# Optimization experiments

Hardware: AMD Instinct MI355X
Metric: run time of the kernel (lower is better)

The kernel has to match this reference:

```python
import jax, jax.numpy as jnp
import numpy as np

H = 128   # hidden_size
E = 300   # embedding_dim
VOC = 32000
B, TP, TC = 8, 160, 160
D2 = 2 * H  # bidirectional feature dim


def gru_dir(x, Wih, Whh, bih, bhh, reverse):
    # x: [B,T,I] -> hidden states [B,T,Hs]; torch GRU gate order (r,z,n)
    Hs = Whh.shape[1]
    xg = jnp.einsum('bti,gi->btg', x, Wih) + bih  # [B,T,3Hs]
    if reverse:
        xg = xg[:, ::-1]
    def step(h, xt):
        gh = h @ Whh.T + bhh
        xr, xz, xn = jnp.split(xt, 3, axis=-1)
        hr, hz, hn = jnp.split(gh, 3, axis=-1)
        r = jax.nn.sigmoid(xr + hr)
        z = jax.nn.sigmoid(xz + hz)
        n = jnp.tanh(xn + r * hn)
        h = (1.0 - z) * n + z * h
        return h, h
    h0 = jnp.zeros((x.shape[0], Hs), x.dtype)
    _, hs = jax.lax.scan(step, h0, jnp.swapaxes(xg, 0, 1))
    hs = jnp.swapaxes(hs, 0, 1)
    if reverse:
        hs = hs[:, ::-1]
    return hs


def bigru(x, Wf, Uf, bif, bhf, Wb, Ub, bib, bhb):
    return jnp.concatenate([
        gru_dir(x, Wf, Uf, bif, bhf, False),
        gru_dir(x, Wb, Ub, bib, bhb, True)], axis=-1)


def setup_inputs() -> dict:
    key = jax.random.key(0)
    ks = iter(jax.random.split(key, 64))
    def rn(shape, s=0.05):
        return jax.random.normal(next(ks), shape, jnp.float32) * s
    inp = {}
    inp['text_a'] = jax.random.randint(next(ks), (B, TP), 0, VOC)
    inp['text_b'] = jax.random.randint(next(ks), (B, TC), 0, VOC)
    inp['emb'] = rn((VOC, E), 0.1)
    for pfx, ins in [('p', E), ('c', E), ('a', 6 * D2)]:
        for d in ('f', 'b'):
            inp[pfx + '_Wih_' + d] = rn((3 * H, ins))
            inp[pfx + '_Whh_' + d] = rn((3 * H, H))
            inp[pfx + '_bih_' + d] = jnp.zeros((3 * H,), jnp.float32)
            inp[pfx + '_bhh_' + d] = jnp.zeros((3 * H,), jnp.float32)
    inp['Wc1'] = rn((H, D2)); inp['Wc2'] = rn((H, D2)); inp['Vc'] = rn((H,))
    inp['Wb'] = rn((D2, D2))
    inp['Wd'] = rn((H, D2)); inp['Vd'] = rn((H,))
    inp['Wm'] = rn((H, D2)); inp['Vm'] = rn((H,))
    inp['Ws'] = rn((H, D2)); inp['Vs'] = rn((H,))
    inp['Wp'] = rn((H, D2)); inp['Vp'] = rn((H,))
    inp['W1'] = rn((H, D2)); inp['W2'] = rn((H, D2)); inp['Vv'] = rn((H,))
    inp['Wout'] = rn((2, D2)); inp['bout'] = jnp.zeros((2,), jnp.float32)
    return inp


def _forward(text_a, text_b, emb,
             p_Wih_f, p_Whh_f, p_bih_f, p_bhh_f, p_Wih_b, p_Whh_b, p_bih_b, p_bhh_b,
             c_Wih_f, c_Whh_f, c_bih_f, c_bhh_f, c_Wih_b, c_Whh_b, c_bih_b, c_bhh_b,
             a_Wih_f, a_Whh_f, a_bih_f, a_bhh_f, a_Wih_b, a_Whh_b, a_bih_b, a_bhh_b,
             Wc1, Wc2, Vc, Wb, Wd, Vd, Wm, Vm, Ws, Vs, Wp, Vp, W1, W2, Vv, Wout, bout):
    hp = bigru(emb[text_a], p_Wih_f, p_Whh_f, p_bih_f, p_bhh_f,
               p_Wih_b, p_Whh_b, p_bih_b, p_bhh_b)          # [B,Tp,2H]
    hc = bigru(emb[text_b], c_Wih_f, c_Whh_f, c_bih_f, c_bhh_f,
               c_Wih_b, c_Whh_b, c_bih_b, c_bhh_b)          # [B,Tc,2H]
    # concat (additive) attention: [B,Tc,Tp,H]
    s = jnp.tanh((hp @ Wc1.T)[:, None] + (hc @ Wc2.T)[:, :, None])
    a_cat = jax.nn.softmax(s @ Vc, axis=2)                   # [B,Tc,Tp]
    concat_rep = jnp.einsum('bct,btd->bcd', a_cat, hp)
    # bilinear attention
    a_bil = jax.nn.softmax(jnp.einsum('bcd,btd->bct', hc, hp @ Wb.T), axis=2)
    bil_rep = jnp.einsum('bct,btd->bcd', a_bil, hp)
    # dot / minus attention on [B,Tc,Tp,2H] broadcasts
    hp4 = hp[:, None]; hc4 = hc[:, :, None]
    a_dot = jax.nn.softmax(jnp.tanh((hp4 * hc4) @ Wd.T) @ Vd, axis=2)
    dot_rep = jnp.einsum('bct,btd->bcd', a_dot, hp)
    a_min = jax.nn.softmax(jnp.tanh((hp4 - hc4) @ Wm.T) @ Vm, axis=2)
    minus_rep = jnp.einsum('bct,btd->bcd', a_min, hp)
    # self attention on hc: [B,Tc,Tc,2H]
    a_self = jax.nn.softmax(jnp.tanh((hc[:, None] * hc[:, :, None]) @ Ws.T) @ Vs, axis=2)
    self_rep = jnp.einsum('bct,btd->bcd', a_self, hc)
    agg_in = jnp.concatenate([hc, self_rep, concat_rep, dot_rep, bil_rep, minus_rep], axis=-1)
    agg = bigru(agg_in, a_Wih_f, a_Whh_f, a_bih_f, a_bhh_f,
                a_Wih_b, a_Whh_b, a_bih_b, a_bhh_b)          # [B,Tc,2H]
    # pooled passage rep
    ap = jax.nn.softmax(jnp.tanh(hp @ Wp.T) @ Vp, axis=-1)   # [B,Tp]
    rp = jnp.einsum('bt,btd->bd', ap, hp)                    # [B,2H]
    # final attention over aggregation (note: no tanh, faithful to source)
    sc = (agg @ W1.T + (rp @ W2.T)[:, None]) @ Vv            # [B,Tc]
    ac = jax.nn.softmax(sc, axis=-1)
    rc = jnp.einsum('bc,bcd->bd', ac, agg)                   # [B,2H]
    return rc @ Wout.T + bout                                # [B,2] logits


def reference(text_a, text_b, emb,
              p_Wih_f, p_Whh_f, p_bih_f, p_bhh_f, p_Wih_b, p_Whh_b, p_bih_b, p_bhh_b,
              c_Wih_f, c_Whh_f, c_bih_f, c_bhh_f, c_Wih_b, c_Whh_b, c_bih_b, c_bhh_b,
              a_Wih_f, a_Whh_f, a_bih_f, a_bhh_f, a_Wih_b, a_Whh_b, a_bih_b, a_bhh_b,
              Wc1, Wc2, Vc, Wb, Wd, Vd, Wm, Vm, Ws, Vs, Wp, Vp, W1, W2, Vv, Wout, bout):
    return _forward(text_a, text_b, emb,
                    p_Wih_f, p_Whh_f, p_bih_f, p_bhh_f, p_Wih_b, p_Whh_b, p_bih_b, p_bhh_b,
                    c_Wih_f, c_Whh_f, c_bih_f, c_bhh_f, c_Wih_b, c_Whh_b, c_bih_b, c_bhh_b,
                    a_Wih_f, a_Whh_f, a_bih_f, a_bhh_f, a_Wih_b, a_Whh_b, a_bih_b, a_bhh_b,
                    Wc1, Wc2, Vc, Wb, Wd, Vd, Wm, Vm, Ws, Vs, Wp, Vp, W1, W2, Vv, Wout, bout)
```

## Files before the change

kernel.cpp:

```cpp
#include <hip/hip_runtime.h>

#define BB 8
#define TT 160
#define EE 300
#define HH 128
#define D2 256
#define G3 384
#define PSTR 40

typedef __attribute__((ext_vector_type(8))) short bf16x8;
typedef __attribute__((ext_vector_type(4))) float floatx4;

__device__ inline float fsigmoid(float x){ return 1.f/(1.f+__expf(-x)); }
__device__ inline float ftanh(float x){ return 2.f*fsigmoid(2.f*x) - 1.f; }

__device__ inline void split2(float x, unsigned short& hi, unsigned short& lo){
  unsigned ux = __float_as_uint(x);
  hi = (unsigned short)(ux>>16);
  float r = x - __uint_as_float(ux & 0xFFFF0000u);
  lo = (unsigned short)(__float_as_uint(r)>>16);
}

__global__ __launch_bounds__(256) void k_embed(const int* ta, const int* tb,
    const float* emb, float* ep, float* ec){
  const int idx = blockIdx.x*256 + threadIdx.x;
  const int per = BB*TT*EE;
  if (idx < per){
    const int e = idx % EE, bt = idx / EE;
    ep[idx] = emb[(long)ta[bt]*EE + e];
  } else {
    const int j = idx - per;
    const int e = j % EE, bt = j / EE;
    ec[j] = emb[(long)tb[bt]*EE + e];
  }
}

__global__ __launch_bounds__(256) void k_splitarr(const float* a, const float* b, int n,
    unsigned short* ahi, unsigned short* alo, unsigned short* bhi, unsigned short* blo){
  const int idx = blockIdx.x*256 + threadIdx.x;
  if (idx < n){
    split2(a[idx], ahi[idx], alo[idx]);
    split2(b[idx], bhi[idx], blo[idx]);
  }
}

struct SplitJob { const float* W; unsigned short* hi; unsigned short* lo; int n; int K; int Kp; };
struct SplitJobs { SplitJob j[12]; };

__global__ __launch_bounds__(256) void k_splitw(SplitJobs jobs){
  const SplitJob J = jobs.j[blockIdx.z];
  const int idx = blockIdx.x*256 + threadIdx.x;
  if (idx >= J.n) return;
  const int row = idx / J.Kp, k = idx - row*J.Kp;
  const float v = (k < J.K) ? J.W[(long)row*J.K + k] : 0.f;
  split2(v, J.hi[idx], J.lo[idx]);
}

struct GemmSJob {
  const float* A; const unsigned short* Whi; const unsigned short* Wlo; const float* bias;
  float* C; int N; int K; int Kp;
};
struct GemmSJobs { GemmSJob j[6]; };

__global__ __launch_bounds__(256) void k_gemmS(GemmSJobs jobs){
  const GemmSJob J = jobs.j[blockIdx.z];
  const int tid = threadIdx.x;
  const int lane = tid & 63, w = tid >> 6;
  const int l15 = lane & 15, q = lane >> 4;
  const int n0 = blockIdx.x * 64;
  if (n0 >= J.N) return;
  const int K = J.K, Kp = J.Kp;
  const long mrow = blockIdx.y*64 + w*16 + l15;
  const float* Arow = J.A + mrow*K;
  floatx4 acc[4];
  #pragma unroll
  for (int t=0;t<4;t++) acc[t] = (floatx4)0.f;
  const int nch = (K+31)>>5;
  for (int kc=0; kc<nch; kc++){
    const int k0 = kc<<5;
    const int kb = k0 + q*8;
    float av[8];
    if (k0+32 <= K){
      const floatx4 a0 = *(const floatx4*)(Arow+kb);
      const floatx4 a1 = *(const floatx4*)(Arow+kb+4);
      av[0]=a0[0];av[1]=a0[1];av[2]=a0[2];av[3]=a0[3];
      av[4]=a1[0];av[5]=a1[1];av[6]=a1[2];av[7]=a1[3];
    } else {
      #pragma unroll
      for (int j=0;j<8;j++){ const int k=kb+j; av[j] = (k<K)? Arow[k] : 0.f; }
    }
    union { bf16x8 v; unsigned short u[8]; } ahi, alo;
    #pragma unroll
    for (int j=0;j<8;j++) split2(av[j], ahi.u[j], alo.u[j]);
    #pragma unroll
    for (int t=0;t<4;t++){
      const int n = n0 + t*16 + l15;
      const long wo = (long)n*Kp + kb;
      union { bf16x8 v; uint4 d; } whi, wlo;
      whi.d = *(const uint4*)(J.Whi + wo);
      wlo.d = *(const uint4*)(J.Wlo + wo);
      acc[t] = __builtin_amdgcn_mfma_f32_16x16x32_bf16(ahi.v, whi.v, acc[t], 0,0,0);
      acc[t] = __builtin_amdgcn_mfma_f32_16x16x32_bf16(ahi.v, wlo.v, acc[t], 0,0,0);
      acc[t] = __builtin_amdgcn_mfma_f32_16x16x32_bf16(alo.v, whi.v, acc[t], 0,0,0);
    }
  }
  const long rbase = blockIdx.y*64 + w*16 + q*4;
  #pragma unroll
  for (int t=0;t<4;t++){
    const int n = n0 + t*16 + l15;
    const float bv = J.bias ? J.bias[n] : 0.f;
    #pragma unroll
    for (int r=0;r<4;r++)
      J.C[(rbase+r)*(long)J.N + n] = acc[t][r] + bv;
  }
}

struct GruJob { const float* xg; const float* Whh; const float* bhh; float* out; int ocol; int rev; };
struct GruJobs { GruJob j[4]; };

__global__ __launch_bounds__(256,1) void k_gru(GruJobs jobs){
  const GruJob J = jobs.j[blockIdx.y];
  const int bi = blockIdx.x;
  const int tid = threadIdx.x;
  const int j = tid >> 1, p = tid & 1;
  __shared__ float h_sh[2][HH];
  float wr[64], wz[64], wn[64];
  {
    const float* r0 = J.Whh + (long)j*HH + p*64;
    const float* z0 = J.Whh + (long)(HH+j)*HH + p*64;
    const float* n0 = J.Whh + (long)(2*HH+j)*HH + p*64;
    #pragma unroll
    for (int k=0;k<64;k+=4){
      *(floatx4*)&wr[k] = *(const floatx4*)(r0+k);
      *(floatx4*)&wz[k] = *(const floatx4*)(z0+k);
      *(floatx4*)&wn[k] = *(const floatx4*)(n0+k);
    }
  }
  float bhr=0.f,bhz=0.f,bhn=0.f, xr=0.f,xz=0.f,xn=0.f;
  if (p==0){
    bhr = J.bhh[j]; bhz = J.bhh[HH+j]; bhn = J.bhh[2*HH+j];
    const int t0 = J.rev ? (TT-1) : 0;
    const float* xgp = J.xg + ((long)bi*TT + t0)*G3;
    xr = xgp[j]; xz = xgp[HH+j]; xn = xgp[2*HH+j];
  }
  ((float*)h_sh)[tid] = 0.f;
  float hreg = 0.f;
  __syncthreads();
  for (int t=0;t<TT;t++){
    const int tt = J.rev ? (TT-1-t) : t;
    const int buf = t & 1;
    const float cxr=xr, cxz=xz, cxn=xn;
    if (p==0 && t+1 < TT){
      const int tn = J.rev ? (TT-2-t) : (t+1);
      const float* xgp = J.xg + ((long)bi*TT + tn)*G3;
      xr = xgp[j]; xz = xgp[HH+j]; xn = xgp[2*HH+j];
    }
    float ar0=0.f,ar1=0.f, az0=0.f,az1=0.f, an0=0.f,an1=0.f;
    #pragma unroll
    for (int k=0;k<64;k+=8){
      const floatx4 h0 = *(const floatx4*)&h_sh[buf][p*64+k];
      const floatx4 h1 = *(const floatx4*)&h_sh[buf][p*64+k+4];
      ar0 += wr[k]*h0[0] + wr[k+1]*h0[1] + wr[k+2]*h0[2] + wr[k+3]*h0[3];
      az0 += wz[k]*h0[0] + wz[k+1]*h0[1] + wz[k+2]*h0[2] + wz[k+3]*h0[3];
      an0 += wn[k]*h0[0] + wn[k+1]*h0[1] + wn[k+2]*h0[2] + wn[k+3]*h0[3];
      ar1 += wr[k+4]*h1[0] + wr[k+5]*h1[1] + wr[k+6]*h1[2] + wr[k+7]*h1[3];
      az1 += wz[k+4]*h1[0] + wz[k+5]*h1[1] + wz[k+6]*h1[2] + wz[k+7]*h1[3];
      an1 += wn[k+4]*h1[0] + wn[k+5]*h1[1] + wn[k+6]*h1[2] + wn[k+7]*h1[3];
    }
    float ar = ar0+ar1, az = az0+az1, an = an0+an1;
    ar += __shfl_xor(ar,1);
    az += __shfl_xor(az,1);
    an += __shfl_xor(an,1);
    if (p==0){
      const float gr = fsigmoid(cxr + ar + bhr);
      const float gz = fsigmoid(cxz + az + bhz);
      const float gn = ftanh  (cxn + gr*(an + bhn));
      const float h = (1.f-gz)*gn + gz*hreg;
      hreg = h;
      h_sh[1-buf][j] = h;
      J.out[((long)bi*TT + tt)*D2 + J.ocol + j] = h;
    }
    __syncthreads();
  }
}

__device__ inline float block_softmax160(float s, int tid, float* red){
  float m = s;
  #pragma unroll
  for (int o=32;o>0;o>>=1) m = fmaxf(m, __shfl_xor(m,o));
  if ((tid&63)==0) red[tid>>6] = m;
  __syncthreads();
  m = fmaxf(fmaxf(red[0],red[1]), fmaxf(red[2],red[3]));
  const float p = (tid<TT) ? __expf(s-m) : 0.f;
  float t = p;
  #pragma unroll
  for (int o=32;o>0;o>>=1) t += __shfl_xor(t,o);
  if ((tid&63)==0) red[4+(tid>>6)] = t;
  __syncthreads();
  const float sum = red[4]+red[5]+red[6]+red[7];
  return p / sum;
}

__device__ inline float block_softmax160_512(float s, int tid, float* red){
  float m = s;
  #pragma unroll
  for (int o=32;o>0;o>>=1) m = fmaxf(m, __shfl_xor(m,o));
  if ((tid&63)==0) red[tid>>6] = m;
  __syncthreads();
  m = red[0];
  #pragma unroll
  for (int i=1;i<8;i++) m = fmaxf(m, red[i]);
  const float p = (tid<TT) ? __expf(s-m) : 0.f;
  float t = p;
  #pragma unroll
  for (int o=32;o>0;o>>=1) t += __shfl_xor(t,o);
  if ((tid&63)==0) red[8+(tid>>6)] = t;
  __syncthreads();
  float sum = red[8];
  #pragma unroll
  for (int i=1;i<8;i++) sum += red[8+i];
  return p / sum;
}

struct PairJob { const unsigned short* Phi; const unsigned short* Plo;
                 const float* Q; const float* W; const float* V; float* a_out; };

__global__ __launch_bounds__(512) void k_pairattn(PairJob j0, PairJob j1){
  const PairJob J = blockIdx.z ? j1 : j0;
  const int b = blockIdx.y, c = blockIdx.x;
  const int tid = threadIdx.x;
  const int lane = tid & 63, w = tid >> 6;
  const int l15 = lane & 15, q = lane >> 4;
  __shared__ unsigned short Pb[2*2*160*PSTR];
  __shared__ float Qs[D2];
  __shared__ float sc_sh[TT];
  __shared__ float red[16];
  if (tid < D2) Qs[tid] = J.Q[((long)b*TT + c)*D2 + tid];
  if (tid < TT) sc_sh[tid] = 0.f;
  const long pbase = (long)b*TT*D2;

  int s_hl[5], s_t[5], s_d4[5];
  #pragma unroll
  for (int r=0;r<5;r++){
    const int idx = tid + r*512;
    const int hl = (idx >= 1280) ? 1 : 0;
    const int e4 = idx - hl*1280;
    s_hl[r] = hl; s_t[r] = e4 >> 3; s_d4[r] = e4 & 7;
  }
  uint2 stg[5];
  #pragma unroll
  for (int r=0;r<5;r++){
    const unsigned short* src = (s_hl[r] ? J.Plo : J.Phi) + pbase + (long)s_t[r]*D2 + s_d4[r]*4;
    stg[r] = *(const uint2*)src;
  }
  const float* Wbase = J.W + (long)(w*16 + l15)*D2;
  floatx4 wv0 = *(const floatx4*)(Wbase + q*8);
  floatx4 wv1 = *(const floatx4*)(Wbase + q*8 + 4);
  #pragma unroll
  for (int r=0;r<5;r++)
    *(uint2*)&Pb[((0*2 + s_hl[r])*160 + s_t[r])*PSTR + s_d4[r]*4] = stg[r];
  __syncthreads();

  floatx4 acc[10];
  #pragma unroll
  for (int nt=0;nt<10;nt++) acc[nt] = (floatx4)0.f;

  for (int kc=0; kc<8; kc++){
    const floatx4 wc0 = wv0, wc1 = wv1;
    if (kc < 7){
      wv0 = *(const floatx4*)(Wbase + (kc+1)*32 + q*8);
      wv1 = *(const floatx4*)(Wbase + (kc+1)*32 + q*8 + 4);
      #pragma unroll
      for (int r=0;r<5;r++){
        const unsigned short* src = (s_hl[r] ? J.Plo : J.Phi) + pbase + (long)s_t[r]*D2 + (kc+1)*32 + s_d4[r]*4;
        stg[r] = *(const uint2*)src;
      }
    }
    const int d0 = kc*32 + q*8;
    const floatx4 q0 = *(const floatx4*)&Qs[d0];
    const floatx4 q1 = *(const floatx4*)&Qs[d0+4];
    union { bf16x8 v; unsigned short u[8]; } ah, al;
    #pragma unroll
    for (int j=0;j<4;j++){
      split2(wc0[j]*q0[j], ah.u[j],   al.u[j]);
      split2(wc1[j]*q1[j], ah.u[4+j], al.u[4+j]);
    }
    const int buf = kc & 1;
    #pragma unroll
    for (int nt=0;nt<10;nt++){
      const int t = nt*16 + l15;
      union { bf16x8 v; } bh, bl;
      bh.v = *(const bf16x8*)&Pb[((buf*2+0)*160 + t)*PSTR + q*8];
      bl.v = *(const bf16x8*)&Pb[((buf*2+1)*160 + t)*PSTR + q*8];
      acc[nt] = __builtin_amdgcn_mfma_f32_16x16x32_bf16(ah.v, bh.v, acc[nt], 0,0,0);
      acc[nt] = __builtin_amdgcn_mfma_f32_16x16x32_bf16(ah.v, bl.v, acc[nt], 0,0,0);
      acc[nt] = __builtin_amdgcn_mfma_f32_16x16x32_bf16(al.v, bh.v, acc[nt], 0,0,0);
    }
    if (kc < 7){
      const int nbuf = 1 - buf;
      #pragma unroll
      for (int r=0;r<5;r++)
        *(uint2*)&Pb[((nbuf*2 + s_hl[r])*160 + s_t[r])*PSTR + s_d4[r]*4] = stg[r];
      __syncthreads();
    }
  }

  float vreg[4];
  #pragma unroll
  for (int r=0;r<4;r++) vreg[r] = J.V[w*16 + q*4 + r];
  #pragma unroll
  for (int nt=0;nt<10;nt++){
    float pp = 0.f;
    #pragma unroll
    for (int r=0;r<4;r++) pp += vreg[r]*ftanh(acc[nt][r]);
    pp += __shfl_xor(pp,16);
    pp += __shfl_xor(pp,32);
    if (q==0) atomicAdd(&sc_sh[nt*16 + l15], pp);
  }
  __syncthreads();
  const float s = (tid<TT)? sc_sh[tid] : -INFINITY;
  const float a = block_softmax160_512(s, tid, red);
  if (tid < TT) J.a_out[((long)b*TT + c)*TT + tid] = a;
}

struct AddJob { const float* up; const float* uc; const float* V; float sgn; float* a_out; };

__global__ __launch_bounds__(256) void k_addattn(AddJob j0, AddJob j1){
  const AddJob J = blockIdx.z ? j1 : j0;
  const int b = blockIdx.y, c = blockIdx.x, tid = threadIdx.x;
  __shared__ float ucc[HH];
  __shared__ float vv[HH];
  __shared__ float red[8];
  if (tid < HH){
    ucc[tid] = J.sgn * J.uc[((long)b*TT + c)*HH + tid];
    vv[tid] = J.V[tid];
  }
  __syncthreads();
  float s = -INFINITY;
  if (tid < TT){
    const float* ur = J.up + ((long)b*TT + tid)*HH;
    float a0 = 0.f;
    #pragma unroll 4
    for (int k=0;k<HH;k++) a0 += vv[k]*ftanh(ur[k]+ucc[k]);
    s = a0;
  }
  const float a = block_softmax160(s, tid, red);
  if (tid < TT) J.a_out[((long)b*TT + c)*TT + tid] = a;
}

__global__ __launch_bounds__(256) void k_bilattn(const float* hc, const float* hpWb, float* a_out){
  const int b = blockIdx.y, c = blockIdx.x, tid = threadIdx.x;
  __shared__ float hcc[D2];
  __shared__ float red[8];
  if (tid < D2) hcc[tid] = hc[((long)b*TT + c)*D2 + tid];
  __syncthreads();
  float s = -INFINITY;
  if (tid < TT){
    const float* pr = hpWb + ((long)b*TT + tid)*D2;
    float a0 = 0.f;
    #pragma unroll 4
    for (int k=0;k<D2;k++) a0 += hcc[k]*pr[k];
    s = a0;
  }
  const float a = block_softmax160(s, tid, red);
  if (tid < TT) a_out[((long)b*TT + c)*TT + tid] = a;
}

__global__ __launch_bounds__(256) void k_rep(const float* hp, const float* hc,
    const float* acat, const float* abil, const float* adot, const float* amin, const float* aself,
    float* aggin){
  const int b = blockIdx.y, c = blockIdx.x, tid = threadIdx.x;
  __shared__ float a5[5][TT];
  {
    const long base = ((long)b*TT + c)*TT;
    for (int i=tid;i<5*TT;i+=256){
      const int which = i/TT, t = i - which*TT;
      const float* p = which==0? acat : which==1? abil : which==2? adot : which==3? amin : aself;
      a5[which][t] = p[base + t];
    }
  }
  __syncthreads();
  const float* hpb = hp + (long)b*TT*D2 + tid;
  const float* hcb = hc + (long)b*TT*D2 + tid;
  float r0=0.f,r1=0.f,r2=0.f,r3=0.f,r4=0.f;
  for (int t=0;t<TT;t++){
    const float vp = hpb[(long)t*D2];
    const float vc = hcb[(long)t*D2];
    r0 += a5[0][t]*vp;
    r1 += a5[1][t]*vp;
    r2 += a5[2][t]*vp;
    r3 += a5[3][t]*vp;
    r4 += a5[4][t]*vc;
  }
  float* o = aggin + ((long)b*TT + c)*(6*D2);
  o[tid]        = hc[((long)b*TT + c)*D2 + tid];
  o[D2 + tid]   = r4;
  o[2*D2 + tid] = r0;
  o[3*D2 + tid] = r2;
  o[4*D2 + tid] = r1;
  o[5*D2 + tid] = r3;
}

__global__ __launch_bounds__(256) void k_tail1(const float* upP, const float* Vp,
    const float* hp, float* rp){
  const int b = blockIdx.x, tid = threadIdx.x;
  __shared__ float vv[HH];
  __shared__ float ap_sh[TT];
  __shared__ float red[8];
  if (tid<HH) vv[tid] = Vp[tid];
  __syncthreads();
  float s = -INFINITY;
  if (tid<TT){
    const float* ur = upP + ((long)b*TT + tid)*HH;
    float a0=0.f;
    #pragma unroll 4
    for (int k=0;k<HH;k++) a0 += vv[k]*ftanh(ur[k]);
    s = a0;
  }
  const float a = block_softmax160(s, tid, red);
  if (tid<TT) ap_sh[tid] = a;
  __syncthreads();
  float acc = 0.f;
  const float* hpb = hp + (long)b*TT*D2 + tid;
  for (int t=0;t<TT;t++) acc += ap_sh[t]*hpb[(long)t*D2];
  rp[b*D2 + tid] = acc;
}

__global__ __launch_bounds__(256) void k_tail2(const float* aggW1, const float* agg, const float* rp,
    const float* W2, const float* Vv, const float* Wout, const float* bout,
    float* out){
  const int b = blockIdx.x, tid = threadIdx.x;
  __shared__ float rpw[HH];
  __shared__ float ac_sh[TT];
  __shared__ float rc_sh[D2];
  __shared__ float red[8];
  if (tid < HH){
    float a0=0.f;
    const float* wr2 = W2 + (long)tid*D2;
    const float* rr = rp + b*D2;
    for (int d=0; d<D2; d++) a0 += wr2[d]*rr[d];
    rpw[tid] = a0;
  }
  __syncthreads();
  float s = -INFINITY;
  if (tid < TT){
    const float* ar = aggW1 + ((long)b*TT + tid)*HH;
    float a0=0.f;
    for (int k=0;k<HH;k++) a0 += Vv[k]*(ar[k] + rpw[k]);
    s = a0;
  }
  const float a = block_softmax160(s, tid, red);
  if (tid < TT) ac_sh[tid] = a;
  __syncthreads();
  float rc=0.f;
  const float* ab = agg + (long)b*TT*D2 + tid;
  for (int t=0;t<TT;t++) rc += ac_sh[t]*ab[(long)t*D2];
  rc_sh[tid] = rc;
  __syncthreads();
  if (tid < 2){
    float o = bout[tid];
    const float* wr = Wout + (long)tid*D2;
    for (int d=0; d<D2; d++) o += wr[d]*rc_sh[d];
    out[b*2 + tid] = o;
  }
}

extern "C" void kernel_launch(void* const* d_in, const int* in_sizes, int n_in,
                              void* d_out, int out_size, void* d_ws, size_t ws_size,
                              hipStream_t stream){
  (void)in_sizes; (void)n_in; (void)out_size; (void)ws_size;
  const int* ta = (const int*)d_in[0];
  const int* tb = (const int*)d_in[1];
  const float* emb = (const float*)d_in[2];
  #define F32(i) ((const float*)d_in[i])

  float* ws = (float*)d_ws;
  float* ep    = ws;
  float* ec    = ep    + 384000;
  float* xg_pf = ec    + 384000;
  float* xg_pb = xg_pf + 491520;
  float* xg_cf = xg_pb + 491520;
  float* xg_cb = xg_cf + 491520;
  float* hp    = xg_cb + 491520;
  float* hc    = hp    + 327680;
  float* up1   = hc    + 327680;
  float* uc2   = up1   + 163840;
  float* ump   = uc2   + 163840;
  float* umc   = ump   + 163840;
  float* upP   = umc   + 163840;
  float* hpWb  = upP   + 163840;
  float* acat  = hpWb  + 327680;
  float* abil  = acat  + 204800;
  float* adot  = abil  + 204800;
  float* amin  = adot  + 204800;
  float* aself = amin  + 204800;
  float* aggin = aself + 204800;
  float* rp    = aggin + 1966080;
  unsigned short* hp_hi = (unsigned short*)(rp + 2048);
  unsigned short* hp_lo = hp_hi + 327680;
  unsigned short* hc_hi = hp_lo + 327680;
  unsigned short* hc_lo = hc_hi + 327680;
  unsigned short* wsp = hc_lo + 327680;
  unsigned short* w3h  = wsp;             unsigned short* w3l  = w3h  + 122880;
  unsigned short* w7h  = w3l  + 122880;   unsigned short* w7l  = w7h  + 122880;
  unsigned short* w11h = w7l  + 122880;   unsigned short* w11l = w11h + 122880;
  unsigned short* w15h = w11l + 122880;   unsigned short* w15l = w15h + 122880;
  unsigned short* w27h = w15l + 122880;   unsigned short* w27l = w27h + 32768;
  unsigned short* w28h = w27l + 32768;    unsigned short* w28l = w28h + 32768;
  unsigned short* w33h = w28l + 32768;    unsigned short* w33l = w33h + 32768;
  unsigned short* w37h = w33l + 32768;    unsigned short* w37l = w37h + 32768;
  unsigned short* w30h = w37l + 32768;    unsigned short* w30l = w30h + 65536;
  unsigned short* w19h = w30l + 65536;    unsigned short* w19l = w19h + 589824;
  unsigned short* w23h = w19l + 589824;   unsigned short* w23l = w23h + 589824;
  unsigned short* w39h = w23l + 589824;   unsigned short* w39l = w39h + 32768;
  float* xg_af = xg_pf;
  float* xg_ab = xg_pb;
  float* agg   = xg_cf;
  float* aggW1 = xg_cb;

  k_embed<<<dim3(3000), dim3(256), 0, stream>>>(ta, tb, emb, ep, ec);
  SplitJobs sj = {};
  sj.j[0]  = {F32(3),  w3h,  w3l,  122880, 300, 320};
  sj.j[1]  = {F32(7),  w7h,  w7l,  122880, 300, 320};
  sj.j[2]  = {F32(11), w11h, w11l, 122880, 300, 320};
  sj.j[3]  = {F32(15), w15h, w15l, 122880, 300, 320};
  sj.j[4]  = {F32(27), w27h, w27l, 32768,  256, 256};
  sj.j[5]  = {F32(28), w28h, w28l, 32768,  256, 256};
  sj.j[6]  = {F32(33), w33h, w33l, 32768,  256, 256};
  sj.j[7]  = {F32(37), w37h, w37l, 32768,  256, 256};
  sj.j[8]  = {F32(30), w30h, w30l, 65536,  256, 256};
  sj.j[9]  = {F32(19), w19h, w19l, 589824, 1536, 1536};
  sj.j[10] = {F32(23), w23h, w23l, 589824, 1536, 1536};
  sj.j[11] = {F32(39), w39h, w39l, 32768,  256, 256};
  k_splitw<<<dim3(2304,1,12), dim3(256), 0, stream>>>(sj);

  GemmSJobs ja = {};
  ja.j[0] = {ep, w3h,  w3l,  F32(5),  xg_pf, 384, 300, 320};
  ja.j[1] = {ep, w7h,  w7l,  F32(9),  xg_pb, 384, 300, 320};
  ja.j[2] = {ec, w11h, w11l, F32(13), xg_cf, 384, 300, 320};
  ja.j[3] = {ec, w15h, w15l, F32(17), xg_cb, 384, 300, 320};
  k_gemmS<<<dim3(6,20,4), dim3(256), 0, stream>>>(ja);

  GruJobs gj = {};
  gj.j[0] = {xg_pf, F32(4),  F32(6),  hp, 0,   0};
  gj.j[1] = {xg_pb, F32(8),  F32(10), hp, 128, 1};
  gj.j[2] = {xg_cf, F32(12), F32(14), hc, 0,   0};
  gj.j[3] = {xg_cb, F32(16), F32(18), hc, 128, 1};
  k_gru<<<dim3(8,4), dim3(256), 0, stream>>>(gj);

  k_splitarr<<<dim3(1280), dim3(256), 0, stream>>>(hp, hc, 327680, hp_hi, hp_lo, hc_hi, hc_lo);

  GemmSJobs jb = {};
  jb.j[0] = {hp, w27h, w27l, nullptr, up1,  128, 256, 256};
  jb.j[1] = {hc, w28h, w28l, nullptr, uc2,  128, 256, 256};
  jb.j[2] = {hp, w33h, w33l, nullptr, ump,  128, 256, 256};
  jb.j[3] = {hc, w33h, w33l, nullptr, umc,  128, 256, 256};
  jb.j[4] = {hp, w37h, w37l, nullptr, upP,  128, 256, 256};
  jb.j[5] = {hp, w30h, w30l, nullptr, hpWb, 256, 256, 256};
  k_gemmS<<<dim3(4,20,6), dim3(256), 0, stream>>>(jb);

  PairJob pd  = {hp_hi, hp_lo, hc, F32(31), F32(32), adot};
  PairJob psf = {hc_hi, hc_lo, hc, F32(35), F32(36), aself};
  k_pairattn<<<dim3(160,8,2), dim3(512), 0, stream>>>(pd, psf);

  AddJob ac_ = {up1, uc2, F32(29),  1.f, acat};
  AddJob am_ = {ump, umc, F32(34), -1.f, amin};
  k_addattn<<<dim3(160,8,2), dim3(256), 0, stream>>>(ac_, am_);

  k_bilattn<<<dim3(160,8), dim3(256), 0, stream>>>(hc, hpWb, abil);

  k_tail1<<<dim3(8), dim3(256), 0, stream>>>(upP, F32(38), hp, rp);

  k_rep<<<dim3(160,8), dim3(256), 0, stream>>>(hp, hc, acat, abil, adot, amin, aself, aggin);

  GemmSJobs jc = {};
  jc.j[0] = {aggin, w19h, w19l, F32(21), xg_af, 384, 1536, 1536};
  jc.j[1] = {aggin, w23h, w23l, F32(25), xg_ab, 384, 1536, 1536};
  k_gemmS<<<dim3(6,20,2), dim3(256), 0, stream>>>(jc);

  GruJobs gja = {};
  gja.j[0] = {xg_af, F32(20), F32(22), agg, 0,   0};
  gja.j[1] = {xg_ab, F32(24), F32(26), agg, 128, 1};
  k_gru<<<dim3(8,2), dim3(256), 0, stream>>>(gja);

  GemmSJobs jd = {};
  jd.j[0] = {agg, w39h, w39l, nullptr, aggW1, 128, 256, 256};
  k_gemmS<<<dim3(2,20,1), dim3(256), 0, stream>>>(jd);

  k_tail2<<<dim3(8), dim3(256), 0, stream>>>(aggW1, agg, rp, F32(40), F32(41), F32(42), F32(43),
                                             (float*)d_out);
  #undef F32
}
```

Before: 868.1 us.

## Split GRU recurrence across 4 lanes per unit and stage xg/h in LDS chunks

The GRU kernel goes from 256 to 512 threads, so each hidden unit's three dot products are split across 4 lanes instead of 2. That halves the serial FMA chain per step but adds a second shuffle-reduction level. The input-gate projections for 16 timesteps are bulk-loaded into shared memory with vectorized loads, replacing the per-step scalar global prefetch. Hidden outputs are buffered in LDS and written back as coalesced float4 stores every 16 steps. The cost is an extra barrier per 16-step chunk and more threads taking part in every per-step __syncthreads.

Result: faster. 835.9 us (-3.7%).

```diff
diff --git a/kernel.cpp b/kernel.cpp
--- a/kernel.cpp
+++ b/kernel.cpp
@@ -118,69 +118,73 @@
 struct GruJob { const float* xg; const float* Whh; const float* bhh; float* out; int ocol; int rev; };
 struct GruJobs { GruJob j[4]; };
 
-__global__ __launch_bounds__(256,1) void k_gru(GruJobs jobs){
+__global__ __launch_bounds__(512,1) void k_gru(GruJobs jobs){
   const GruJob J = jobs.j[blockIdx.y];
   const int bi = blockIdx.x;
   const int tid = threadIdx.x;
-  const int j = tid >> 1, p = tid & 1;
-  __shared__ float h_sh[2][HH];
-  float wr[64], wz[64], wn[64];
+  const int j = tid >> 2, p = tid & 3;
+  __shared__ float xgt[16][G3];
+  __shared__ float hbuf[16][HH];
+  __shared__ float hcur[2][HH];
+  float wr[32], wz[32], wn[32];
   {
-    const float* r0 = J.Whh + (long)j*HH + p*64;
-    const float* z0 = J.Whh + (long)(HH+j)*HH + p*64;
-    const float* n0 = J.Whh + (long)(2*HH+j)*HH + p*64;
-    #pragma unroll
-    for (int k=0;k<64;k+=4){
+    const float* r0 = J.Whh + (long)j*HH + p*32;
+    const float* z0 = J.Whh + (long)(HH+j)*HH + p*32;
+    const float* n0 = J.Whh + (long)(2*HH+j)*HH + p*32;
+    #pragma unroll
+    for (int k=0;k<32;k+=4){
       *(floatx4*)&wr[k] = *(const floatx4*)(r0+k);
       *(floatx4*)&wz[k] = *(const floatx4*)(z0+k);
       *(floatx4*)&wn[k] = *(const floatx4*)(n0+k);
     }
   }
-  float bhr=0.f,bhz=0.f,bhn=0.f, xr=0.f,xz=0.f,xn=0.f;
-  if (p==0){
-    bhr = J.bhh[j]; bhz = J.bhh[HH+j]; bhn = J.bhh[2*HH+j];
-    const int t0 = J.rev ? (TT-1) : 0;
-    const float* xgp = J.xg + ((long)bi*TT + t0)*G3;
-    xr = xgp[j]; xz = xgp[HH+j]; xn = xgp[2*HH+j];
-  }
-  ((float*)h_sh)[tid] = 0.f;
+  float bhr=0.f,bhz=0.f,bhn=0.f;
+  if (p==0){ bhr = J.bhh[j]; bhz = J.bhh[HH+j]; bhn = J.bhh[2*HH+j]; }
+  if (tid < 256) ((float*)hcur)[tid] = 0.f;
   float hreg = 0.f;
   __syncthreads();
-  for (int t=0;t<TT;t++){
-    const int tt = J.rev ? (TT-1-t) : t;
-    const int buf = t & 1;
-    const float cxr=xr, cxz=xz, cxn=xn;
-    if (p==0 && t+1 < TT){
-      const int tn = J.rev ? (TT-2-t) : (t+1);
-      const float* xgp = J.xg + ((long)bi*TT + tn)*G3;
-      xr = xgp[j]; xz = xgp[HH+j]; xn = xgp[2*HH+j];
-    }
-    float ar0=0.f,ar1=0.f, az0=0.f,az1=0.f, an0=0.f,an1=0.f;
-    #pragma unroll
-    for (int k=0;k<64;k+=8){
-      const floatx4 h0 = *(const floatx4*)&h_sh[buf][p*64+k];
-      const floatx4 h1 = *(const floatx4*)&h_sh[buf][p*64+k+4];
-      ar0 += wr[k]*h0[0] + wr[k+1]*h0[1] + wr[k+2]*h0[2] + wr[k+3]*h0[3];
-      az0 += wz[k]*h0[0] + wz[k+1]*h0[1] + wz[k+2]*h0[2] + wz[k+3]*h0[3];
-      an0 += wn[k]*h0[0] + wn[k+1]*h0[1] + wn[k+2]*h0[2] + wn[k+3]*h0[3];
-      ar1 += wr[k+4]*h1[0] + wr[k+5]*h1[1] + wr[k+6]*h1[2] + wr[k+7]*h1[3];
-      az1 += wz[k+4]*h1[0] + wz[k+5]*h1[1] + wz[k+6]*h1[2] + wz[k+7]*h1[3];
-      an1 += wn[k+4]*h1[0] + wn[k+5]*h1[1] + wn[k+6]*h1[2] + wn[k+7]*h1[3];
-    }
-    float ar = ar0+ar1, az = az0+az1, an = an0+an1;
-    ar += __shfl_xor(ar,1);
-    az += __shfl_xor(az,1);
-    an += __shfl_xor(an,1);
-    if (p==0){
-      const float gr = fsigmoid(cxr + ar + bhr);
-      const float gz = fsigmoid(cxz + az + bhz);
-      const float gn = ftanh  (cxn + gr*(an + bhn));
-      const float h = (1.f-gz)*gn + gz*hreg;
-      hreg = h;
-      h_sh[1-buf][j] = h;
-      J.out[((long)bi*TT + tt)*D2 + J.ocol + j] = h;
+
+  for (int s0=0; s0<TT; s0+=16){
+    #pragma unroll
+    for (int r=0;r<3;r++){
+      const int i = r*512 + tid;
+      const int row = i/96, c4 = i - row*96;
+      const int tt = J.rev ? (TT-1-(s0+row)) : (s0+row);
+      *(floatx4*)&xgt[row][c4*4] = *(const floatx4*)(J.xg + ((long)bi*TT + tt)*G3 + c4*4);
     }
     __syncthreads();
+    for (int si=0; si<16; si++){
+      const int s = s0 + si;
+      const int buf = s & 1;
+      float cxr=0.f,cxz=0.f,cxn=0.f;
+      if (p==0){ cxr = xgt[si][j]; cxz = xgt[si][HH+j]; cxn = xgt[si][2*HH+j]; }
+      float ar=0.f, az=0.f, an=0.f;
+      #pragma unroll
+      for (int k=0;k<32;k+=4){
+        const floatx4 h4 = *(const floatx4*)&hcur[buf][p*32+k];
+        ar += wr[k]*h4[0] + wr[k+1]*h4[1] + wr[k+2]*h4[2] + wr[k+3]*h4[3];
+        az += wz[k]*h4[0] + wz[k+1]*h4[1] + wz[k+2]*h4[2] + wz[k+3]*h4[3];
+        an += wn[k]*h4[0] + wn[k+1]*h4[1] + wn[k+2]*h4[2] + wn[k+3]*h4[3];
+      }
+      ar += __shfl_xor(ar,1); ar += __shfl_xor(ar,2);
+      az += __shfl_xor(az,1); az += __shfl_xor(az,2);
+      an += __shfl_xor(an,1); an += __shfl_xor(an,2);
+      if (p==0){
+        const float gr = fsigmoid(cxr + ar + bhr);
+        const float gz = fsigmoid(cxz + az + bhz);
+        const float gn = ftanh  (cxn + gr*(an + bhn));
+        const float h = (1.f-gz)*gn + gz*hreg;
+        hreg = h;
+        hcur[1-buf][j] = h;
+        hbuf[si][j] = h;
+      }
+      __syncthreads();
+    }
+    {
+      const int row = tid >> 5, c4 = tid & 31;
+      const int tt = J.rev ? (TT-1-(s0+row)) : (s0+row);
+      *(floatx4*)(J.out + ((long)bi*TT + tt)*D2 + J.ocol + c4*4) = *(const floatx4*)&hbuf[row][c4*4];
+    }
   }
 }
 
@@ -546,7 +550,7 @@
   gj.j[1] = {xg_pb, F32(8),  F32(10), hp, 128, 1};
   gj.j[2] = {xg_cf, F32(12), F32(14), hc, 0,   0};
   gj.j[3] = {xg_cb, F32(16), F32(18), hc, 128, 1};
-  k_gru<<<dim3(8,4), dim3(256), 0, stream>>>(gj);
+  k_gru<<<dim3(8,4), dim3(512), 0, stream>>>(gj);
 
   k_splitarr<<<dim3(1280), dim3(256), 0, stream>>>(hp, hc, 327680, hp_hi, hp_lo, hc_hi, hc_lo);
 
@@ -581,7 +585,7 @@
   GruJobs gja = {};
   gja.j[0] = {xg_af, F32(20), F32(22), agg, 0,   0};
   gja.j[1] = {xg_ab, F32(24), F32(26), agg, 128, 1};
-  k_gru<<<dim3(8,2), dim3(256), 0, stream>>>(gja);
+  k_gru<<<dim3(8,2), dim3(512), 0, stream>>>(gja);
 
   GemmSJobs jd = {};
   jd.j[0] = {agg, w39h, w39l, nullptr, aggW1, 128, 256, 256};
```
